# Performance work log

Measured on AMD Instinct MI355X. Metric: run time of the kernel, lower is better.

## Reference

```python
import jax, jax.numpy as jnp
import numpy as np

D_MODEL = 1024
NHEAD = 16
D_HEAD = D_MODEL // NHEAD
D_FF = 4096
B, S = 2, 2048
EPS = 1e-5


def _linear_params(key, d_in, d_out):
    kw, kb = jax.random.split(key)
    bound = 1.0 / np.sqrt(d_in)
    W = jax.random.uniform(kw, (d_out, d_in), jnp.float32, -bound, bound)
    b = jax.random.uniform(kb, (d_out,), jnp.float32, -bound, bound)
    return W, b


def setup_inputs() -> dict:
    key = jax.random.key(0)
    ks = jax.random.split(key, 8)
    x = jax.random.normal(ks[0], (B, S, D_MODEL), jnp.float32)
    Wq, bq = _linear_params(ks[1], D_MODEL, D_MODEL)
    Wk, bk = _linear_params(ks[2], D_MODEL, D_MODEL)
    Wv, bv = _linear_params(ks[3], D_MODEL, D_MODEL)
    Wo, bo = _linear_params(ks[4], D_MODEL, D_MODEL)
    W1, b1 = _linear_params(ks[5], D_MODEL, D_FF)
    W2, b2 = _linear_params(ks[6], D_FF, D_MODEL)
    g1 = jnp.ones((D_MODEL,), jnp.float32); be1 = jnp.zeros((D_MODEL,), jnp.float32)
    g2 = jnp.ones((D_MODEL,), jnp.float32); be2 = jnp.zeros((D_MODEL,), jnp.float32)
    return dict(x=x, Wq=Wq, bq=bq, Wk=Wk, bk=bk, Wv=Wv, bv=bv, Wo=Wo, bo=bo,
                W1=W1, b1=b1, W2=W2, b2=b2, g1=g1, be1=be1, g2=g2, be2=be2)


def _layernorm(x, g, b):
    mu = jnp.mean(x, axis=-1, keepdims=True)
    var = jnp.mean(jnp.square(x - mu), axis=-1, keepdims=True)
    return (x - mu) * jax.lax.rsqrt(var + EPS) * g + b


def reference(x, Wq, bq, Wk, bk, Wv, bv, Wo, bo, W1, b1, W2, b2, g1, be1, g2, be2):
    b_, s_, _ = x.shape
    # QKV projections (nn.Linear: x @ W.T + b)
    q = x @ Wq.T + bq
    k = x @ Wk.T + bk
    v = x @ Wv.T + bv
    # split heads -> [b, h, s, d_head]
    qh = q.reshape(b_, s_, NHEAD, D_HEAD).transpose(0, 2, 1, 3)
    kh = k.reshape(b_, s_, NHEAD, D_HEAD).transpose(0, 2, 1, 3)
    vh = v.reshape(b_, s_, NHEAD, D_HEAD).transpose(0, 2, 1, 3)
    scores = jnp.einsum('bhqd,bhkd->bhqk', qh, kh) / jnp.sqrt(jnp.float32(D_HEAD))
    attn_w = jax.nn.softmax(scores, axis=-1)
    attn_out = jnp.einsum('bhqk,bhkd->bhqd', attn_w, vh)
    attn_concat = attn_out.transpose(0, 2, 1, 3).reshape(b_, s_, D_MODEL)
    attn_proj = attn_concat @ Wo.T + bo
    # residual + LN1
    h = _layernorm(x + attn_proj, g1, be1)
    # FFN
    ffn = jax.nn.relu(h @ W1.T + b1) @ W2.T + b2
    # residual + LN2
    return _layernorm(h + ffn, g2, be2)
```

## Files before the change

kernel.cpp:

```cpp
#include <hip/hip_runtime.h>
#include <hip/hip_bf16.h>

#define D_MODEL 1024
#define NHEAD 16
#define D_HEAD 64
#define D_FF 4096
#define BATCH 2
#define SEQ 2048
#define M_TOK (BATCH * SEQ)
#define EPS 1e-5f
#define QKV_N 3072

using bf16 = __hip_bfloat16;
typedef __attribute__((ext_vector_type(8))) short short8;
typedef __attribute__((ext_vector_type(4))) short short4v;
typedef __attribute__((ext_vector_type(4))) float float4v;
typedef __attribute__((ext_vector_type(16))) float float16v;

__device__ __forceinline__ float b2f(unsigned short u) {
    union { unsigned int i; float f; } v; v.i = ((unsigned int)u) << 16; return v.f;
}
__device__ __forceinline__ unsigned short f2b(float f) {
    union { float f; unsigned int u; } v; v.f = f;
    unsigned int r = v.u + 0x7FFFu + ((v.u >> 16) & 1u);
    return (unsigned short)(r >> 16);
}
__device__ __forceinline__ float loadAt(const void* p, size_t i, int f32) {
    if (f32) return ((const float*)p)[i];
    return b2f(((const unsigned short*)p)[i]);
}
__device__ __forceinline__ void async16(const void* g, void* lds) {
    __builtin_amdgcn_global_load_lds(
        (const __attribute__((address_space(1))) unsigned int*)g,
        (__attribute__((address_space(3))) unsigned int*)lds, 16, 0, 0);
}

__global__ void detect_kernel(const unsigned short* __restrict__ x, int* __restrict__ flag) {
    __shared__ int cnt;
    if (threadIdx.x == 0) cnt = 0;
    __syncthreads();
    int c = 0;
    for (int i = threadIdx.x; i < 8192; i += 256) {
        unsigned short u = x[i];
        int e = (u >> 7) & 0xFF;
        if (e >= 0xF0) c++;
    }
    atomicAdd(&cnt, c);
    __syncthreads();
    if (threadIdx.x == 0) { flag[0] = (cnt > 16) ? 1 : 0; flag[1] = 0; }
}

__global__ __launch_bounds__(256) void cast_bf16_kernel(
    const void* __restrict__ src, bf16* __restrict__ dst, int n,
    const int* __restrict__ flagp) {
    const int f32 = *flagp;
    int i0 = (blockIdx.x * 256 + threadIdx.x) * 8;
    if (i0 >= n) return;
    short8 v;
    if (f32) {
        const float* pf = (const float*)src + i0;
        float4v f0 = *(const float4v*)pf;
        float4v f1 = *(const float4v*)(pf + 4);
#pragma unroll
        for (int i = 0; i < 4; i++) { v[i] = (short)f2b(f0[i]); v[4 + i] = (short)f2b(f1[i]); }
    } else {
        v = *(const short8*)((const short*)src + i0);
    }
    *(short8*)((short*)dst + i0) = v;
}

__global__ __launch_bounds__(256) void cast3_bf16_kernel(
    const void* __restrict__ s0, const void* __restrict__ s1,
    const void* __restrict__ s2, bf16* __restrict__ dst,
    const int* __restrict__ flagp) {
    const int f32 = *flagp;
    int i0 = (blockIdx.x * 256 + threadIdx.x) * 8;
    const int part = i0 >> 20;
    const int off = i0 & ((1 << 20) - 1);
    const void* src = (part == 0) ? s0 : (part == 1) ? s1 : s2;
    short8 v;
    if (f32) {
        const float* pf = (const float*)src + off;
        float4v f0 = *(const float4v*)pf;
        float4v f1 = *(const float4v*)(pf + 4);
#pragma unroll
        for (int i = 0; i < 4; i++) { v[i] = (short)f2b(f0[i]); v[4 + i] = (short)f2b(f1[i]); }
    } else {
        v = *(const short8*)((const short*)src + off);
    }
    *(short8*)((short*)dst + i0) = v;
}

__global__ __launch_bounds__(256) void cast2_bf16_kernel(
    const void* __restrict__ s0, const void* __restrict__ s1,
    bf16* __restrict__ d0, bf16* __restrict__ d1,
    const int* __restrict__ flagp) {
    const int f32 = *flagp;
    int i0 = (blockIdx.x * 256 + threadIdx.x) * 8;
    const void* src; short* dst; int off;
    if (i0 < (1 << 20)) { src = s0; dst = (short*)d0; off = i0; }
    else                { src = s1; dst = (short*)d1; off = i0 - (1 << 20); }
    short8 v;
    if (f32) {
        const float* pf = (const float*)src + off;
        float4v f0 = *(const float4v*)pf;
        float4v f1 = *(const float4v*)(pf + 4);
#pragma unroll
        for (int i = 0; i < 4; i++) { v[i] = (short)f2b(f0[i]); v[4 + i] = (short)f2b(f1[i]); }
    } else {
        v = *(const short8*)((const short*)src + off);
    }
    *(short8*)(dst + off) = v;
}

__device__ __forceinline__ void stage8(const void* src, size_t off, int f32, short* dst) {
    short8 v;
    if (f32) {
        const float* pf = (const float*)src + off;
        float4v f0 = *(const float4v*)pf;
        float4v f1 = *(const float4v*)(pf + 4);
#pragma unroll
        for (int i = 0; i < 4; i++) { v[i] = (short)f2b(f0[i]); v[4 + i] = (short)f2b(f1[i]); }
    } else {
        v = *(const short8*)((const short*)src + off);
    }
    *(short8*)dst = v;
}

template <int MF, int NF, bool RELU, bool BDYN>
__global__ __launch_bounds__(256) void gemm_mfma(
    const bf16* __restrict__ A, const void* __restrict__ B,
    const void* __restrict__ bias0, const void* __restrict__ bias1,
    const void* __restrict__ bias2, int nb1, int nb2,
    bf16* __restrict__ C, int N, int K, const int* __restrict__ inFlagp) {
    constexpr int BM = 32 * MF, BN = 32 * NF;
    __shared__ short As[BM * 64];
    __shared__ short Bs[BN * 64];
    const int tid = threadIdx.x;
    const int lane = tid & 63;
    const int wv = tid >> 6;
    const int wm = wv & 1, wn = wv >> 1;
    const int quad = lane >> 4, lrow = lane & 15;
    const int rowM = blockIdx.y * BM;
    const int rowN = blockIdx.x * BN;
    const int inf = *inFlagp;

    float4v acc[MF][NF];
    const float4v zero = {0.f, 0.f, 0.f, 0.f};
#pragma unroll
    for (int i = 0; i < MF; i++)
#pragma unroll
        for (int j = 0; j < NF; j++) acc[i][j] = zero;

    const int sRow = lane >> 3;
    const int gChunk = (lane & 7) ^ sRow;

    for (int k0 = 0; k0 < K; k0 += 64) {
#pragma unroll
        for (int rd = 0; rd < MF; rd++) {
            const short* gp = (const short*)A +
                (size_t)(rowM + rd * 32 + wv * 8 + sRow) * K + k0 + gChunk * 8;
            async16(gp, &As[rd * 2048 + wv * 512]);
        }
        if (!BDYN) {
#pragma unroll
            for (int rd = 0; rd < NF; rd++) {
                const short* gp = (const short*)B +
                    (size_t)(rowN + rd * 32 + wv * 8 + sRow) * K + k0 + gChunk * 8;
                async16(gp, &Bs[rd * 2048 + wv * 512]);
            }
        } else {
            const int brow = tid >> 2;
            const int c0 = (tid & 3) * 2;
#pragma unroll
            for (int cc = 0; cc < 2; cc++) {
                int slot = c0 + cc;
                int g = slot ^ (brow & 7);
                stage8(B, (size_t)(rowN + brow) * K + k0 + g * 8, inf,
                       &Bs[brow * 64 + slot * 8]);
            }
        }
        __syncthreads();
#pragma unroll
        for (int ks = 0; ks < 2; ks++) {
            short8 a_frag[MF], b_frag[NF];
#pragma unroll
            for (int i = 0; i < MF; i++) {
                const int row = wm * MF * 16 + i * 16 + lrow;
                const int slot = (ks * 4 + quad) ^ (row & 7);
                a_frag[i] = *(const short8*)&As[row * 64 + slot * 8];
            }
#pragma unroll
            for (int j = 0; j < NF; j++) {
                const int row = wn * NF * 16 + j * 16 + lrow;
                const int slot = (ks * 4 + quad) ^ (row & 7);
                b_frag[j] = *(const short8*)&Bs[row * 64 + slot * 8];
            }
#pragma unroll
            for (int i = 0; i < MF; i++)
#pragma unroll
                for (int j = 0; j < NF; j++)
                    acc[i][j] = __builtin_amdgcn_mfma_f32_16x16x32_bf16(
                        a_frag[i], b_frag[j], acc[i][j], 0, 0, 0);
        }
        __syncthreads();
    }

    const int mB = rowM + wm * MF * 16, nB = rowN + wn * NF * 16;
    unsigned short* Cu = (unsigned short*)C;
#pragma unroll
    for (int j = 0; j < NF; j++) {
        const int col = nB + j * 16 + lrow;
        float bv;
        if (col < nb1)      bv = loadAt(bias0, col, inf);
        else if (col < nb2) bv = loadAt(bias1, col - nb1, inf);
        else                bv = loadAt(bias2, col - nb2, inf);
#pragma unroll
        for (int i = 0; i < MF; i++) {
#pragma unroll
            for (int r = 0; r < 4; r++) {
                const int rowg = mB + i * 16 + quad * 4 + r;
                float vv = acc[i][j][r] + bv;
                if (RELU) vv = fmaxf(vv, 0.0f);
                Cu[(size_t)rowg * N + col] = f2b(vv);
            }
        }
    }
}

#define FSTRIDE 66
__global__ __launch_bounds__(256) void flash_attn_kernel(
    const bf16* __restrict__ Qb, const bf16* __restrict__ Kb,
    const bf16* __restrict__ Vb, bf16* __restrict__ O) {
    const int bid = blockIdx.x;
    const int qt = bid & 15;
    const int h  = (bid >> 4) & 15;
    const int b  = bid >> 8;
    const int q0 = qt * 128;
    const int tid = threadIdx.x;
    const int lane = tid & 63;
    const int wv = tid >> 6;
    const int half = lane >> 5;
    const int l31 = lane & 31;

    __shared__ short Ab[128 * FSTRIDE];
    __shared__ short Ks[2][64 * 64];
    __shared__ short Vt[2][64 * FSTRIDE];

    const size_t headOff = (size_t)h * D_HEAD;
    const float SCF = 0.18033688f;

    {
        int r = tid >> 1, c0 = (tid & 1) * 32;
        const short* src = (const short*)Qb + (size_t)(b * SEQ + q0 + r) * QKV_N + headOff + c0;
#pragma unroll
        for (int ch = 0; ch < 4; ch++) {
            short8 v = *(const short8*)(src + ch * 8);
            short8 o;
#pragma unroll
            for (int e = 0; e < 8; e++)
                o[e] = (short)f2b(b2f((unsigned short)v[e]) * SCF);
            *(short8*)&Ab[r * FSTRIDE + c0 + ch * 8] = o;
        }
    }

    const int sRow = lane >> 3;
    const int gChunk = (lane & 7) ^ sRow;
    const int vjp = (tid & 31) * 2;
    const int vd0 = (tid >> 5) * 8;

#pragma unroll
    for (int rd = 0; rd < 2; rd++) {
        const short* gp = (const short*)Kb +
            (size_t)(b * SEQ + rd * 32 + wv * 8 + sRow) * QKV_N + headOff + gChunk * 8;
        async16(gp, &Ks[0][(rd * 32 + wv * 8) * 64]);
    }
    short8 v0, v1;
    {
        const short* s0 = (const short*)Vb + (size_t)(b * SEQ + vjp) * QKV_N + headOff + vd0;
        v0 = *(const short8*)s0;
        v1 = *(const short8*)(s0 + QKV_N);
    }
    __syncthreads();

    short8 a_q[4];
#pragma unroll
    for (int ks = 0; ks < 4; ks++)
        a_q[ks] = *(const short8*)&Ab[(wv * 32 + l31) * FSTRIDE + ks * 16 + half * 8];

#pragma unroll
    for (int e = 0; e < 8; e++) {
        unsigned int wa = (unsigned int)(unsigned short)v0[e] |
                          ((unsigned int)(unsigned short)v1[e] << 16);
        *(unsigned int*)&Vt[0][(vd0 + e) * FSTRIDE + vjp] = wa;
    }
    __syncthreads();

    float16v o_acc[2];
    float lsum[16];
#pragma unroll
    for (int i = 0; i < 16; i++) { o_acc[0][i] = 0.f; o_acc[1][i] = 0.f; lsum[i] = 0.f; }

    int cb = 0;
    for (int t = 0; t < SEQ / 64; t++) {
        const int jn = (t < SEQ / 64 - 1) ? (t + 1) * 64 : t * 64;
#pragma unroll
        for (int rd = 0; rd < 2; rd++) {
            const short* gp = (const short*)Kb +
                (size_t)(b * SEQ + jn + rd * 32 + wv * 8 + sRow) * QKV_N + headOff + gChunk * 8;
            async16(gp, &Ks[cb ^ 1][(rd * 32 + wv * 8) * 64]);
        }
        {
            const short* s0 = (const short*)Vb + (size_t)(b * SEQ + jn + vjp) * QKV_N + headOff + vd0;
            v0 = *(const short8*)s0;
            v1 = *(const short8*)(s0 + QKV_N);
        }

        float16v s_acc[2];
#pragma unroll
        for (int i = 0; i < 16; i++) { s_acc[0][i] = 0.f; s_acc[1][i] = 0.f; }
#pragma unroll
        for (int ks = 0; ks < 4; ks++)
#pragma unroll
            for (int jb = 0; jb < 2; jb++) {
                const int row = jb * 32 + l31;
                const int slot = (ks * 2 + half) ^ (l31 & 7);
                short8 bfr = *(const short8*)&Ks[cb][row * 64 + slot * 8];
                s_acc[jb] = __builtin_amdgcn_mfma_f32_32x32x16_bf16(a_q[ks], bfr, s_acc[jb], 0, 0, 0);
            }

#pragma unroll
        for (int jb = 0; jb < 2; jb++)
#pragma unroll
            for (int reg = 0; reg < 16; reg++) {
                float pv = exp2f(s_acc[jb][reg]);
                lsum[reg] += pv;
                union { float f; unsigned int u; } uu; uu.f = pv;
                const int rowC = (reg & 3) + 8 * (reg >> 2) + 4 * half;
                Ab[(wv * 32 + rowC) * FSTRIDE + jb * 32 + l31] = (short)(uu.u >> 16);
            }

#pragma unroll
        for (int ks = 0; ks < 4; ks++) {
            short8 pa = *(const short8*)&Ab[(wv * 32 + l31) * FSTRIDE + ks * 16 + half * 8];
#pragma unroll
            for (int db = 0; db < 2; db++) {
                short8 vbf = *(const short8*)&Vt[cb][(db * 32 + l31) * FSTRIDE + ks * 16 + half * 8];
                o_acc[db] = __builtin_amdgcn_mfma_f32_32x32x16_bf16(pa, vbf, o_acc[db], 0, 0, 0);
            }
        }

#pragma unroll
        for (int e = 0; e < 8; e++) {
            unsigned int wa = (unsigned int)(unsigned short)v0[e] |
                              ((unsigned int)(unsigned short)v1[e] << 16);
            *(unsigned int*)&Vt[cb ^ 1][(vd0 + e) * FSTRIDE + vjp] = wa;
        }
        __syncthreads();
        cb ^= 1;
    }

    float invl[16];
#pragma unroll
    for (int reg = 0; reg < 16; reg++) {
        float t = lsum[reg];
        t += __shfl_xor(t, 1);
        t += __shfl_xor(t, 2);
        t += __shfl_xor(t, 4);
        t += __shfl_xor(t, 8);
        t += __shfl_xor(t, 16);
        invl[reg] = 1.0f / t;
    }
    unsigned short* Ou = (unsigned short*)O;
#pragma unroll
    for (int db = 0; db < 2; db++)
#pragma unroll
        for (int reg = 0; reg < 16; reg++) {
            const int rowC = (reg & 3) + 8 * (reg >> 2) + 4 * half;
            const int rowg = b * SEQ + q0 + wv * 32 + rowC;
            Ou[(size_t)rowg * D_MODEL + headOff + db * 32 + l31] =
                f2b(o_acc[db][reg] * invl[reg]);
        }
}

template <bool OUT_F32>
__global__ __launch_bounds__(256) void add_ln_kernel(
    const void* __restrict__ X, const bf16* __restrict__ R,
    const void* __restrict__ g, const void* __restrict__ be,
    void* __restrict__ Y,
    const int* __restrict__ xFlagp, const int* __restrict__ wFlagp) {
    const int xf = *xFlagp;
    const int wf = *wFlagp;
    const int row = blockIdx.x;
    const size_t base = (size_t)row * D_MODEL;
    const int tid = threadIdx.x;
    const int i0 = tid * 4;
    __shared__ float red[256];
    float v[4];
    if (xf) {
        float4v xv = *(const float4v*)((const float*)X + base + i0);
        short4v rv = *(const short4v*)((const short*)R + base + i0);
#pragma unroll
        for (int i = 0; i < 4; i++) v[i] = xv[i] + b2f((unsigned short)rv[i]);
    } else {
        short4v xv = *(const short4v*)((const short*)X + base + i0);
        short4v rv = *(const short4v*)((const short*)R + base + i0);
#pragma unroll
        for (int i = 0; i < 4; i++) v[i] = b2f((unsigned short)xv[i]) + b2f((unsigned short)rv[i]);
    }
    float s = v[0] + v[1] + v[2] + v[3];
    red[tid] = s; __syncthreads();
    for (int s2 = 128; s2 > 0; s2 >>= 1) {
        if (tid < s2) red[tid] += red[tid + s2];
        __syncthreads();
    }
    float mu = red[0] * (1.0f / D_MODEL);
    __syncthreads();
    float s2v = 0.f;
#pragma unroll
    for (int i = 0; i < 4; i++) { float dd = v[i] - mu; s2v += dd * dd; }
    red[tid] = s2v; __syncthreads();
    for (int s2 = 128; s2 > 0; s2 >>= 1) {
        if (tid < s2) red[tid] += red[tid + s2];
        __syncthreads();
    }
    float rstd = rsqrtf(red[0] * (1.0f / D_MODEL) + EPS);
    float gv[4], bv[4];
    if (wf) {
        float4v gg = *(const float4v*)((const float*)g + i0);
        float4v bb = *(const float4v*)((const float*)be + i0);
#pragma unroll
        for (int i = 0; i < 4; i++) { gv[i] = gg[i]; bv[i] = bb[i]; }
    } else {
        short4v gg = *(const short4v*)((const short*)g + i0);
        short4v bb = *(const short4v*)((const short*)be + i0);
#pragma unroll
        for (int i = 0; i < 4; i++) { gv[i] = b2f((unsigned short)gg[i]); bv[i] = b2f((unsigned short)bb[i]); }
    }
    if (OUT_F32) {
        float4v o;
#pragma unroll
        for (int i = 0; i < 4; i++) o[i] = (v[i] - mu) * rstd * gv[i] + bv[i];
        *(float4v*)((float*)Y + base + i0) = o;
    } else {
        short4v o;
#pragma unroll
        for (int i = 0; i < 4; i++) o[i] = (short)f2b((v[i] - mu) * rstd * gv[i] + bv[i]);
        *(short4v*)((short*)Y + base + i0) = o;
    }
}

extern "C" void kernel_launch(void* const* d_in, const int* in_sizes, int n_in,
                              void* d_out, int out_size, void* d_ws, size_t ws_size,
                              hipStream_t stream) {
    const void* x  = d_in[0];
    const void* Wq = d_in[1];  const void* bq = d_in[2];
    const void* Wk = d_in[3];  const void* bk = d_in[4];
    const void* Wv = d_in[5];  const void* bv = d_in[6];
    const void* Wo = d_in[7];  const void* bo = d_in[8];
    const void* W1 = d_in[9];  const void* b1 = d_in[10];
    const void* W2 = d_in[11]; const void* b2 = d_in[12];
    const void* g1 = d_in[13]; const void* be1 = d_in[14];
    const void* g2 = d_in[15]; const void* be2 = d_in[16];

    char* ws = (char*)d_ws;
    const size_t MB = 1024 * 1024;
    bf16* xb     = (bf16*)(ws + 0 * MB);
    bf16* wqkvb  = (bf16*)(ws + 8 * MB);
    bf16* wob    = (bf16*)(ws + 14 * MB);
    bf16* qkv    = (bf16*)(ws + 16 * MB);
    bf16* concat = (bf16*)(ws + 40 * MB);
    bf16* w1b    = (bf16*)(ws + 0 * MB);
    bf16* proj   = (bf16*)(ws + 16 * MB);
    bf16* hb     = (bf16*)(ws + 8 * MB);
    bf16* ffn1   = (bf16*)(ws + 16 * MB);
    bf16* ffn2   = (bf16*)(ws + 0 * MB);
    const bool castW2 = (ws_size >= 56 * MB + 8);
    bf16* w2b    = (bf16*)(ws + 48 * MB);
    int*  flag   = (int*)(ws + (castW2 ? 56 * MB : 48 * MB));

    const int* fIn = flag;
    const int* fBf = flag + 1;

    dim3 blk(256);

    detect_kernel<<<dim3(1), blk, 0, stream>>>((const unsigned short*)x, flag);
    cast_bf16_kernel<<<dim3((M_TOK * D_MODEL / 8 + 255) / 256), blk, 0, stream>>>(x, xb, M_TOK * D_MODEL, fIn);
    cast3_bf16_kernel<<<dim3(3 * D_MODEL * D_MODEL / 8 / 256), blk, 0, stream>>>(Wq, Wk, Wv, wqkvb, fIn);
    if (castW2)
        cast_bf16_kernel<<<dim3((D_FF * D_MODEL / 8 + 255) / 256), blk, 0, stream>>>(W2, w2b, D_FF * D_MODEL, fIn);
    gemm_mfma<4, 4, false, false><<<dim3(QKV_N / 128, M_TOK / 128), blk, 0, stream>>>(
        xb, wqkvb, bq, bk, bv, 1024, 2048, qkv, QKV_N, D_MODEL, fIn);
    cast2_bf16_kernel<<<dim3(5 * D_MODEL * D_MODEL / 8 / 256), blk, 0, stream>>>(Wo, W1, wob, w1b, fIn);
    flash_attn_kernel<<<dim3(BATCH * NHEAD * (SEQ / 128)), dim3(256), 0, stream>>>(
        qkv, qkv + D_MODEL, qkv + 2 * D_MODEL, concat);
    gemm_mfma<2, 2, false, false><<<dim3(D_MODEL / 64, M_TOK / 64), blk, 0, stream>>>(
        concat, wob, bo, bo, bo, D_MODEL, D_MODEL, proj, D_MODEL, D_MODEL, fIn);
    add_ln_kernel<false><<<dim3(M_TOK), blk, 0, stream>>>(x, proj, g1, be1, hb, fIn, fIn);
    gemm_mfma<4, 4, true, false><<<dim3(D_FF / 128, M_TOK / 128), blk, 0, stream>>>(
        hb, w1b, b1, b1, b1, D_FF, D_FF, ffn1, D_FF, D_MODEL, fIn);
    if (castW2)
        gemm_mfma<2, 2, false, false><<<dim3(D_MODEL / 64, M_TOK / 64), blk, 0, stream>>>(
            ffn1, w2b, b2, b2, b2, D_MODEL, D_MODEL, ffn2, D_MODEL, D_FF, fIn);
    else
        gemm_mfma<2, 2, false, true><<<dim3(D_MODEL / 64, M_TOK / 64), blk, 0, stream>>>(
            ffn1, W2, b2, b2, b2, D_MODEL, D_MODEL, ffn2, D_MODEL, D_FF, fIn);
    add_ln_kernel<true><<<dim3(M_TOK), blk, 0, stream>>>(hb, ffn2, g2, be2, d_out, fBf, fIn);
}
```

Before: 380.7 us.

## Keep attention probabilities in registers via transposed QK MFMA and permlane swap

The QK^T MFMA now takes its operands in swapped order, so each lane holds a column of S^T. The exp'd probabilities are packed to bf16 with v_cvt_pk_bf16 and rearranged with v_permlane32_swap into the A-operand layout for the PV MFMA. This removes the LDS write/read round trip for P and collapses the row-sum to one scalar per lane, reduced with a single shuffle at the end. s_setprio hints are also added around the MFMA blocks, and rounding changes from truncation to the hardware convert.

```diff
diff --git a/kernel.cpp b/kernel.cpp
--- a/kernel.cpp
+++ b/kernel.cpp
@@ -33,6 +33,14 @@
     __builtin_amdgcn_global_load_lds(
         (const __attribute__((address_space(1))) unsigned int*)g,
         (__attribute__((address_space(3))) unsigned int*)lds, 16, 0, 0);
+}
+__device__ __forceinline__ unsigned int cvt_pk_bf16(float lo, float hi) {
+    unsigned int r;
+    asm("v_cvt_pk_bf16_f32 %0, %1, %2" : "=v"(r) : "v"(lo), "v"(hi));
+    return r;
+}
+__device__ __forceinline__ void pl32_swap(unsigned int& a, unsigned int& b) {
+    asm("v_permlane32_swap_b32 %0, %1" : "+v"(a), "+v"(b));
 }
 
 __global__ void detect_kernel(const unsigned short* __restrict__ x, int* __restrict__ flag) {
@@ -297,9 +305,9 @@
     __syncthreads();
 
     float16v o_acc[2];
-    float lsum[16];
-#pragma unroll
-    for (int i = 0; i < 16; i++) { o_acc[0][i] = 0.f; o_acc[1][i] = 0.f; lsum[i] = 0.f; }
+#pragma unroll
+    for (int i = 0; i < 16; i++) { o_acc[0][i] = 0.f; o_acc[1][i] = 0.f; }
+    float lsum = 0.f;
 
     int cb = 0;
     for (int t = 0; t < SEQ / 64; t++) {
@@ -319,36 +327,53 @@
         float16v s_acc[2];
 #pragma unroll
         for (int i = 0; i < 16; i++) { s_acc[0][i] = 0.f; s_acc[1][i] = 0.f; }
+        __builtin_amdgcn_s_setprio(1);
 #pragma unroll
         for (int ks = 0; ks < 4; ks++)
 #pragma unroll
             for (int jb = 0; jb < 2; jb++) {
                 const int row = jb * 32 + l31;
                 const int slot = (ks * 2 + half) ^ (l31 & 7);
-                short8 bfr = *(const short8*)&Ks[cb][row * 64 + slot * 8];
-                s_acc[jb] = __builtin_amdgcn_mfma_f32_32x32x16_bf16(a_q[ks], bfr, s_acc[jb], 0, 0, 0);
-            }
+                short8 kfr = *(const short8*)&Ks[cb][row * 64 + slot * 8];
+                s_acc[jb] = __builtin_amdgcn_mfma_f32_32x32x16_bf16(kfr, a_q[ks], s_acc[jb], 0, 0, 0);
+            }
+        __builtin_amdgcn_s_setprio(0);
 
 #pragma unroll
         for (int jb = 0; jb < 2; jb++)
 #pragma unroll
             for (int reg = 0; reg < 16; reg++) {
                 float pv = exp2f(s_acc[jb][reg]);
-                lsum[reg] += pv;
-                union { float f; unsigned int u; } uu; uu.f = pv;
-                const int rowC = (reg & 3) + 8 * (reg >> 2) + 4 * half;
-                Ab[(wv * 32 + rowC) * FSTRIDE + jb * 32 + l31] = (short)(uu.u >> 16);
-            }
-
+                s_acc[jb][reg] = pv;
+                lsum += pv;
+            }
+
+        short8 pa[4];
+#pragma unroll
+        for (int jb = 0; jb < 2; jb++)
+#pragma unroll
+            for (int c = 0; c < 2; c++) {
+                unsigned int a0 = cvt_pk_bf16(s_acc[jb][8 * c + 0], s_acc[jb][8 * c + 1]);
+                unsigned int a1 = cvt_pk_bf16(s_acc[jb][8 * c + 2], s_acc[jb][8 * c + 3]);
+                unsigned int b0 = cvt_pk_bf16(s_acc[jb][8 * c + 4], s_acc[jb][8 * c + 5]);
+                unsigned int b1 = cvt_pk_bf16(s_acc[jb][8 * c + 6], s_acc[jb][8 * c + 7]);
+                pl32_swap(a0, b0);
+                pl32_swap(a1, b1);
+                union { unsigned int w[4]; short8 s; } u;
+                u.w[0] = a0; u.w[1] = a1; u.w[2] = b0; u.w[3] = b1;
+                pa[jb * 2 + c] = u.s;
+            }
+
+        __builtin_amdgcn_s_setprio(1);
 #pragma unroll
         for (int ks = 0; ks < 4; ks++) {
-            short8 pa = *(const short8*)&Ab[(wv * 32 + l31) * FSTRIDE + ks * 16 + half * 8];
 #pragma unroll
             for (int db = 0; db < 2; db++) {
                 short8 vbf = *(const short8*)&Vt[cb][(db * 32 + l31) * FSTRIDE + ks * 16 + half * 8];
-                o_acc[db] = __builtin_amdgcn_mfma_f32_32x32x16_bf16(pa, vbf, o_acc[db], 0, 0, 0);
-            }
-        }
+                o_acc[db] = __builtin_amdgcn_mfma_f32_32x32x16_bf16(pa[ks], vbf, o_acc[db], 0, 0, 0);
+            }
+        }
+        __builtin_amdgcn_s_setprio(0);
 
 #pragma unroll
         for (int e = 0; e < 8; e++) {
@@ -360,27 +385,18 @@
         cb ^= 1;
     }
 
-    float invl[16];
+    const float ltot = lsum + __shfl_xor(lsum, 32);
+    unsigned short* Ou = (unsigned short*)O;
 #pragma unroll
     for (int reg = 0; reg < 16; reg++) {
-        float t = lsum[reg];
-        t += __shfl_xor(t, 1);
-        t += __shfl_xor(t, 2);
-        t += __shfl_xor(t, 4);
-        t += __shfl_xor(t, 8);
-        t += __shfl_xor(t, 16);
-        invl[reg] = 1.0f / t;
-    }
-    unsigned short* Ou = (unsigned short*)O;
-#pragma unroll
-    for (int db = 0; db < 2; db++)
-#pragma unroll
-        for (int reg = 0; reg < 16; reg++) {
-            const int rowC = (reg & 3) + 8 * (reg >> 2) + 4 * half;
-            const int rowg = b * SEQ + q0 + wv * 32 + rowC;
+        const int rowC = (reg & 3) + 8 * (reg >> 2) + 4 * half;
+        const float invl = 1.0f / __shfl(ltot, rowC);
+        const int rowg = b * SEQ + q0 + wv * 32 + rowC;
+#pragma unroll
+        for (int db = 0; db < 2; db++)
             Ou[(size_t)rowg * D_MODEL + headOff + db * 32 + l31] =
-                f2b(o_acc[db][reg] * invl[reg]);
-        }
+                f2b(o_acc[db][reg] * invl);
+    }
 }
 
 template <bool OUT_F32>
```

New measurement: 383.5 us. No clear change (+0.7%).
